# Kernel tuning notes

Hardware: AMD Instinct MI355X
Metric: run time of the kernel (lower is better)

The kernel has to match this reference:

```python
import jax, jax.numpy as jnp
import numpy as np

EMBED_DIM = 512  # channels C
B, H, W = 2, 64, 64


def _conv1x1(x, w, b):
    # x: [B, C, H, W]; w: [C_out, C_in]; b: [C_out]  (1x1 conv == per-pixel linear)
    return jnp.einsum('bchw,dc->bdhw', x, w) + b[None, :, None, None]


def setup_inputs() -> dict:
    key = jax.random.key(0)
    ks = jax.random.split(key, 9)
    C = EMBED_DIM
    s = 1.0 / np.sqrt(C)
    x = jax.random.normal(ks[0], (B, C, H, W), dtype=jnp.float32)
    wq = jax.random.normal(ks[1], (C, C), dtype=jnp.float32) * s
    bq = jax.random.normal(ks[2], (C,), dtype=jnp.float32) * 0.01
    wk = jax.random.normal(ks[3], (C, C), dtype=jnp.float32) * s
    bk = jax.random.normal(ks[4], (C,), dtype=jnp.float32) * 0.01
    wv = jax.random.normal(ks[5], (C, C), dtype=jnp.float32) * s
    bv = jax.random.normal(ks[6], (C,), dtype=jnp.float32) * 0.01
    wo = jax.random.normal(ks[7], (C, C), dtype=jnp.float32) * s
    bo = jax.random.normal(ks[8], (C,), dtype=jnp.float32) * 0.01
    return {"x": x, "wq": wq, "bq": bq, "wk": wk, "bk": bk,
            "wv": wv, "bv": bv, "wo": wo, "bo": bo}


def reference(x, wq, bq, wk, bk, wv, bv, wo, bo):
    b, c, h, w = x.shape
    n = h * w
    q = _conv1x1(x, wq, bq).reshape(b, c, n)
    k = _conv1x1(x, wk, bk).reshape(b, c, n)
    v = _conv1x1(x, wv, bv).reshape(b, c, n)
    # scores = q^T @ k over channel dim -> [b, n, n]; scale by sqrt(C) (scale=True)
    scores = jnp.einsum('bcn,bcm->bnm', q, k) / jnp.sqrt(jnp.asarray(c, x.dtype))
    attn = jax.nn.softmax(scores, axis=-1)
    # output = v @ attn^T -> [b, c, n]
    out = jnp.einsum('bcm,bnm->bcn', v, attn).reshape(b, c, h, w)
    return _conv1x1(out, wo, bo)
```

## Files before the change

### kernel.cpp

```cpp
#include <hip/hip_runtime.h>
#include <stdint.h>

typedef short s16x8 __attribute__((ext_vector_type(8)));
typedef unsigned short u16x8 __attribute__((ext_vector_type(8)));
typedef float f32x4 __attribute__((ext_vector_type(4)));

__device__ __forceinline__ float bf2f(unsigned short u) {
  union { unsigned u; float f; } c; c.u = ((unsigned)u) << 16; return c.f;
}
__device__ __forceinline__ unsigned short f2bf(float f) {
  union { float f; unsigned u; } c; c.f = f;
  unsigned u = c.u + 0x7fffu + ((c.u >> 16) & 1u);
  return (unsigned short)(u >> 16);
}

__device__ __forceinline__ void g2l16(const void* g, void* l) {
  __builtin_amdgcn_global_load_lds(
      (const __attribute__((address_space(1))) void*)(unsigned long long)g,
      (__attribute__((address_space(3))) void*)(unsigned)(unsigned long long)l,
      16, 0, 0);
}

template <int MODE, int MT, int YB>
__global__ __launch_bounds__(2 * MT) void gemm_abt(
    const unsigned short* __restrict__ A, int lda,
    const unsigned short* __restrict__ Bt, int ldb,
    unsigned short* __restrict__ C, int ldc,
    const float* __restrict__ bias,
    float* __restrict__ rowsum,
    int M, int N, int K, int nsplit,
    long long sA, long long sBt, long long sC, long long sSplit,
    float scale)
{
  constexpr int STAGE_ELEMS  = (MT + 128) * 64;
  constexpr int BOUNCE_ELEMS = 128 * 136;
  constexpr int SMEM_ELEMS = STAGE_ELEMS > BOUNCE_ELEMS ? STAGE_ELEMS : BOUNCE_ELEMS;
  __shared__ __align__(16) unsigned short smem[SMEM_ELEMS];
  unsigned short* As = smem;
  unsigned short* Bs = smem + MT * 64;

  const int ks = blockIdx.z % nsplit;
  const int bz = blockIdx.z / nsplit;
  A  += (long long)bz * sA;
  Bt += (long long)bz * sBt;
  C  += (long long)bz * sC + (long long)ks * sSplit;

  int bx, by;
  if (YB > 0) {
    const int lin = blockIdx.x + (int)gridDim.x * blockIdx.y;
    bx = (lin & 7) | ((lin >> (3 + YB)) << 3);
    by = (lin >> 3) & ((1 << YB) - 1);
  } else {
    bx = blockIdx.x;
    by = blockIdx.y;
  }

  const int tile_m = by * MT;
  const int tile_n = bx * 128;

  const int tid  = threadIdx.x;
  const int wid  = tid >> 6;
  const int lane = tid & 63;
  const int wm = (wid >> 1) * 64;
  const int wn = (wid & 1) * 64;
  const int lr = lane & 15;
  const int lq = lane >> 4;

  const int srow = lane >> 3;
  const int scol = ((lane & 7) ^ (srow & 7)) * 8;

  f32x4 acc[4][4];
  const f32x4 zero4 = {0.f, 0.f, 0.f, 0.f};
  #pragma unroll
  for (int i = 0; i < 4; ++i)
    #pragma unroll
    for (int j = 0; j < 4; ++j) acc[i][j] = zero4;

  const unsigned short* Arow = A  + (long long)tile_m * lda;
  const unsigned short* Brow = Bt + (long long)tile_n * ldb;

  const int kLen = K / nsplit;
  const int kBeg = ks * kLen;

  constexpr int ACH   = MT / 8;
  constexpr int NCH   = ACH + 16;
  constexpr int NW    = MT / 32;
  constexpr int PERW  = NCH / NW;

  for (int k0 = kBeg; k0 < kBeg + kLen; k0 += 64) {
    #pragma unroll
    for (int c = 0; c < PERW; ++c) {
      const int chunk = wid * PERW + c;
      if (chunk < ACH) {
        const int row = chunk * 8 + srow;
        g2l16(Arow + (long long)row * lda + k0 + scol, smem + chunk * 512);
      } else {
        const int row = (chunk - ACH) * 8 + srow;
        g2l16(Brow + (long long)row * ldb + k0 + scol, smem + chunk * 512);
      }
    }
    __syncthreads();
    #pragma unroll
    for (int kss = 0; kss < 2; ++kss) {
      const int cch = kss * 4 + lq;
      s16x8 af[4], bfr[4];
      #pragma unroll
      for (int i = 0; i < 4; ++i) {
        const int row = wm + i * 16 + lr;
        af[i] = *(const s16x8*)&As[row * 64 + ((cch ^ (row & 7)) * 8)];
      }
      #pragma unroll
      for (int j = 0; j < 4; ++j) {
        const int row = wn + j * 16 + lr;
        bfr[j] = *(const s16x8*)&Bs[row * 64 + ((cch ^ (row & 7)) * 8)];
      }
      #pragma unroll
      for (int i = 0; i < 4; ++i)
        #pragma unroll
        for (int j = 0; j < 4; ++j)
          acc[i][j] = __builtin_amdgcn_mfma_f32_16x16x32_bf16(af[i], bfr[j], acc[i][j], 0, 0, 0);
    }
    __syncthreads();
  }

  if (MODE == 2) {
    #pragma unroll
    for (int i = 0; i < 4; ++i) {
      float rs[4] = {0.f, 0.f, 0.f, 0.f};
      #pragma unroll
      for (int j = 0; j < 4; ++j)
        #pragma unroll
        for (int r = 0; r < 4; ++r) {
          acc[i][j][r] = __expf(acc[i][j][r] * scale);
          rs[r] += acc[i][j][r];
        }
      #pragma unroll
      for (int r = 0; r < 4; ++r) {
        float s = rs[r];
        s += __shfl_xor(s, 1); s += __shfl_xor(s, 2);
        s += __shfl_xor(s, 4); s += __shfl_xor(s, 8);
        if (lr == 0)
          atomicAdd(&rowsum[(long long)bz * M + tile_m + wm + i * 16 + lq * 4 + r], s);
      }
    }
  }

  if (MT == 128) {
    #pragma unroll
    for (int i = 0; i < 4; ++i) {
      const int lrow0 = wm + i * 16 + lq * 4;
      #pragma unroll
      for (int j = 0; j < 4; ++j) {
        const int lcol = wn + j * 16 + lr;
        const float bcol = (MODE == 1 && bias) ? bias[tile_n + lcol] : 0.f;
        #pragma unroll
        for (int r = 0; r < 4; ++r) {
          const float v = (MODE == 2) ? acc[i][j][r] : acc[i][j][r] * scale + bcol;
          smem[(lrow0 + r) * 136 + lcol] = f2bf(v);
        }
      }
    }
    __syncthreads();
    const int row = tid >> 1;
    const int cb = (tid & 1) * 64;
    #pragma unroll
    for (int k = 0; k < 8; ++k) {
      u16x8 v = *(const u16x8*)&smem[row * 136 + cb + k * 8];
      *(u16x8*)&C[(long long)(tile_m + row) * ldc + tile_n + cb + k * 8] = v;
    }
  } else {
    #pragma unroll
    for (int p = 0; p < 2; ++p) {
      if ((wm >> 7) == p) {
        const int lwm = wm & 127;
        #pragma unroll
        for (int i = 0; i < 4; ++i) {
          const int lrow0 = lwm + i * 16 + lq * 4;
          #pragma unroll
          for (int j = 0; j < 4; ++j) {
            const int lcol = wn + j * 16 + lr;
            const float bcol = (MODE == 1 && bias) ? bias[tile_n + lcol] : 0.f;
            #pragma unroll
            for (int r = 0; r < 4; ++r) {
              const float v = (MODE == 2) ? acc[i][j][r] : acc[i][j][r] * scale + bcol;
              smem[(lrow0 + r) * 136 + lcol] = f2bf(v);
            }
          }
        }
      }
      __syncthreads();
      if ((tid >> 8) == p) {
        const int t2 = tid & 255;
        const int row = t2 >> 1;
        const int cb = (t2 & 1) * 64;
        #pragma unroll
        for (int k = 0; k < 8; ++k) {
          u16x8 v = *(const u16x8*)&smem[row * 136 + cb + k * 8];
          *(u16x8*)&C[(long long)(tile_m + p * 128 + row) * ldc + tile_n + cb + k * 8] = v;
        }
      }
      if (p == 0) __syncthreads();
    }
  }
}

__global__ __launch_bounds__(256) void cvt_weights(
    const float* __restrict__ wq, const float* __restrict__ wk,
    const float* __restrict__ wv, const float* __restrict__ wo,
    const float* __restrict__ bq, const float* __restrict__ bk,
    const float* __restrict__ bv, const float* __restrict__ bo,
    unsigned short* __restrict__ W3, unsigned short* __restrict__ wvT_b,
    unsigned short* __restrict__ wo_b, float* __restrict__ bqk3,
    float* __restrict__ bpp, float* __restrict__ rowsum, int n)
{
  if ((int)blockIdx.x < 1024) {
    const int i = blockIdx.x * 256 + threadIdx.x;
    if (i < n) {
      W3[i]      = f2bf(wq[i]);
      W3[n + i]  = f2bf(wk[i]);
      wvT_b[i]   = f2bf(wv[(i & 511) * 512 + (i >> 9)]);
      wo_b[i]    = f2bf(wo[i]);
    }
    if (i < 512) {
      bqk3[i]        = bq[i];
      bqk3[512 + i]  = bk[i];
      bqk3[1024 + i] = 0.f;
    }
    if (i < 8192) rowsum[i] = 0.f;
  } else {
    const int w = threadIdx.x >> 6, lane = threadIdx.x & 63;
    const int d = (blockIdx.x - 1024) * 4 + w;
    const float* row = wo + (long long)d * 512;
    float s = 0.f;
    #pragma unroll
    for (int c = 0; c < 512; c += 64) s += row[c + lane] * bv[c + lane];
    #pragma unroll
    for (int o = 32; o > 0; o >>= 1) s += __shfl_xor(s, o, 64);
    if (lane == 0) bpp[d] = s + bo[d];
  }
}

__global__ __launch_bounds__(256) void transpose_cn(
    const float* __restrict__ x, unsigned short* __restrict__ xT,
    int C, int N)
{
  __shared__ float tile[32][33];
  const long long boff = (long long)blockIdx.z * C * N;
  const int n0 = blockIdx.x * 32;
  const int c0 = blockIdx.y * 32;
  const int tx = threadIdx.x;
  const int ty = threadIdx.y;
  #pragma unroll
  for (int k = 0; k < 32; k += 8)
    tile[ty + k][tx] = x[boff + (long long)(c0 + ty + k) * N + n0 + tx];
  __syncthreads();
  #pragma unroll
  for (int k = 0; k < 32; k += 8)
    xT[boff + (long long)(n0 + ty + k) * C + c0 + tx] = f2bf(tile[tx][ty + k]);
}

__global__ __launch_bounds__(256) void transpose_bf(
    const unsigned short* __restrict__ src, int srcLd, long long sSrc,
    unsigned short* __restrict__ dst, int dstLd, long long sDst,
    int R, int Cc)
{
  __shared__ unsigned short tile[32][33];
  const int r0 = blockIdx.x * 32;
  const int c0 = blockIdx.y * 32;
  const int tx = threadIdx.x;
  const int ty = threadIdx.y;
  const long long so = (long long)blockIdx.z * sSrc;
  const long long dofs = (long long)blockIdx.z * sDst;
  #pragma unroll
  for (int k = 0; k < 32; k += 8)
    tile[ty + k][tx] = src[so + (long long)(r0 + ty + k) * srcLd + c0 + tx];
  __syncthreads();
  #pragma unroll
  for (int k = 0; k < 32; k += 8)
    dst[dofs + (long long)(c0 + ty + k) * dstLd + r0 + tx] = tile[tx][ty + k];
}

__global__ __launch_bounds__(256) void reduce4_norm_out(
    const unsigned short* __restrict__ p, long long L,
    const float* __restrict__ rowsum, const float* __restrict__ bpp,
    float* __restrict__ o)
{
  const long long i = 8LL * (blockIdx.x * 256 + threadIdx.x);
  const int b = (int)(i >> 21);
  const int d = (int)((i >> 12) & 511);
  const int n = (int)(i & 4095);
  const float bb = bpp[d];
  const float* rs = &rowsum[b * 4096 + n];
  u16x8 a  = *(const u16x8*)&p[i];
  u16x8 b1 = *(const u16x8*)&p[L + i];
  u16x8 c  = *(const u16x8*)&p[2 * L + i];
  u16x8 d1 = *(const u16x8*)&p[3 * L + i];
  f32x4 o0, o1;
  #pragma unroll
  for (int j = 0; j < 4; ++j) {
    o0[j] = ((bf2f(a[j]) + bf2f(b1[j])) + (bf2f(c[j]) + bf2f(d1[j]))) / rs[j] + bb;
    o1[j] = ((bf2f(a[4 + j]) + bf2f(b1[4 + j])) + (bf2f(c[4 + j]) + bf2f(d1[4 + j]))) / rs[4 + j] + bb;
  }
  *(f32x4*)&o[i] = o0;
  *(f32x4*)&o[i + 4] = o1;
}

extern "C" void kernel_launch(void* const* d_in, const int* in_sizes, int n_in,
                              void* d_out, int out_size, void* d_ws, size_t ws_size,
                              hipStream_t stream) {
  (void)in_sizes; (void)n_in; (void)out_size; (void)ws_size;
  const float* x  = (const float*)d_in[0];
  const float* wq = (const float*)d_in[1];
  const float* bq = (const float*)d_in[2];
  const float* wk = (const float*)d_in[3];
  const float* bk = (const float*)d_in[4];
  const float* wv = (const float*)d_in[5];
  const float* bv = (const float*)d_in[6];
  const float* wo = (const float*)d_in[7];
  const float* bo = (const float*)d_in[8];
  float* out = (float*)d_out;

  const int Cc = 512, N = 4096, Bn = 2, C3 = 1536;
  const int CC = Cc * Cc;
  const long long NC  = (long long)N * Cc;
  const long long NC3 = (long long)N * C3;
  const long long NN  = (long long)N * N;

  char* wsb = (char*)d_ws;
  unsigned short* W3    = (unsigned short*)wsb;
  unsigned short* wvT_b = W3 + 3LL * CC;
  unsigned short* wo_b  = wvT_b + CC;
  float*          bqk3  = (float*)(wo_b + CC);
  float*          bpp   = bqk3 + 1536;
  float*          rsum  = bpp + 512;
  unsigned short* xT    = (unsigned short*)(rsum + 8192);
  unsigned short* qkvoT = xT + Bn * NC;
  unsigned short* vo    = qkvoT + Bn * NC3;
  unsigned short* S     = vo + Bn * NC;
  unsigned short* part  = S + Bn * NN;

  const float inv_sqrt_c = 0.044194173824159216f;

  cvt_weights<<<dim3(1152), 256, 0, stream>>>(
      wq, wk, wv, wo, bq, bk, bv, bo, W3, wvT_b, wo_b, bqk3, bpp, rsum, CC);
  gemm_abt<1, 128, 0><<<dim3(4, 4, 1), 256, 0, stream>>>(
      wo_b, 512, wvT_b, 512, W3 + 2LL * CC, 512, nullptr, nullptr,
      512, 512, 512, 1, 0, 0, 0, 0, 1.0f);
  transpose_cn<<<dim3(N / 32, Cc / 32, Bn), dim3(32, 8), 0, stream>>>(x, xT, Cc, N);

  gemm_abt<1, 256, 0><<<dim3(C3 / 128, N / 256, Bn), 512, 0, stream>>>(
      xT, Cc, W3, Cc, qkvoT, C3, bqk3, nullptr, N, C3, Cc, 1,
      NC, 0, NC3, 0, 1.0f);
  transpose_bf<<<dim3(N / 32, Cc / 32, Bn), dim3(32, 8), 0, stream>>>(
      qkvoT + 1024, C3, NC3, vo, N, NC, N, Cc);
  gemm_abt<2, 256, 4><<<dim3(N / 128, N / 256, Bn), 512, 0, stream>>>(
      qkvoT, C3, qkvoT + 512, C3, S, N, nullptr, rsum, N, N, Cc, 1,
      NC3, NC3, NN, 0, inv_sqrt_c);
  gemm_abt<1, 256, 1><<<dim3(N / 128, 512 / 256, Bn * 4), 512, 0, stream>>>(
      vo, N, S, N, part, N, nullptr, nullptr, 512, N, N, 4,
      NC, NN, NC, (long long)Bn * NC, 1.0f);
  reduce4_norm_out<<<dim3((int)((Bn * NC) / 2048)), 256, 0, stream>>>(
      part, (long long)Bn * NC, rsum, bpp, out);
}
```

Before: 240.3 us.

## Fuse V transpose into QKV GEMM epilogue and merge prep kernels

The QKV projection GEMM gets a new mode in which tiles covering the V columns are written transposed, through shared memory, straight into the channel-major V buffer. This removes the separate bf16 transpose kernel and its extra read and write of V. The weight conversion and the x transpose are merged into one prep kernel, which saves a launch. Q and K now go to a narrower buffer with stride 1024, and the V tiles skip the bias, which is folded into bpp downstream.

```diff
diff --git a/kernel.cpp b/kernel.cpp
--- a/kernel.cpp
+++ b/kernel.cpp
@@ -3,6 +3,7 @@
 
 typedef short s16x8 __attribute__((ext_vector_type(8)));
 typedef unsigned short u16x8 __attribute__((ext_vector_type(8)));
+typedef unsigned short u16x4 __attribute__((ext_vector_type(4)));
 typedef float f32x4 __attribute__((ext_vector_type(4)));
 
 __device__ __forceinline__ float bf2f(unsigned short u) {
@@ -30,7 +31,8 @@
     float* __restrict__ rowsum,
     int M, int N, int K, int nsplit,
     long long sA, long long sBt, long long sC, long long sSplit,
-    float scale)
+    float scale,
+    unsigned short* __restrict__ C2, int ldc2, long long sC2)
 {
   constexpr int STAGE_ELEMS  = (MT + 128) * 64;
   constexpr int BOUNCE_ELEMS = 128 * 136;
@@ -123,6 +125,42 @@
     __syncthreads();
   }
 
+
+  if (MODE == 3 && bx >= 8) {
+    const int tile_d0 = (bx - 8) * 128;
+    unsigned short* V = C2 + (long long)bz * sC2;
+    #pragma unroll
+    for (int p = 0; p < 2; ++p) {
+      if ((wid & 1) == p) {
+        #pragma unroll
+        for (int j = 0; j < 4; ++j) {
+          const int dl = j * 16 + lr;
+          #pragma unroll
+          for (int i = 0; i < 4; ++i) {
+            const int nbase = wm + i * 16 + lq * 4;
+            u16x4 w4;
+            #pragma unroll
+            for (int r = 0; r < 4; ++r) w4[r] = f2bf(acc[i][j][r]);
+            *(u16x4*)&smem[dl * 264 + nbase] = w4;
+          }
+        }
+      }
+      __syncthreads();
+      {
+        const int dl = tid >> 3;
+        const int nb = (tid & 7) * 32;
+        unsigned short* dst = V + (long long)(tile_d0 + p * 64 + dl) * ldc2 + tile_m + nb;
+        #pragma unroll
+        for (int k = 0; k < 4; ++k) {
+          u16x8 v = *(const u16x8*)&smem[dl * 264 + nb + k * 8];
+          *(u16x8*)&dst[k * 8] = v;
+        }
+      }
+      if (p == 0) __syncthreads();
+    }
+    return;
+  }
+
   if (MODE == 2) {
     #pragma unroll
     for (int i = 0; i < 4; ++i) {
@@ -152,7 +190,7 @@
       #pragma unroll
       for (int j = 0; j < 4; ++j) {
         const int lcol = wn + j * 16 + lr;
-        const float bcol = (MODE == 1 && bias) ? bias[tile_n + lcol] : 0.f;
+        const float bcol = ((MODE == 1 || MODE == 3) && bias) ? bias[tile_n + lcol] : 0.f;
         #pragma unroll
         for (int r = 0; r < 4; ++r) {
           const float v = (MODE == 2) ? acc[i][j][r] : acc[i][j][r] * scale + bcol;
@@ -179,7 +217,7 @@
           #pragma unroll
           for (int j = 0; j < 4; ++j) {
             const int lcol = wn + j * 16 + lr;
-            const float bcol = (MODE == 1 && bias) ? bias[tile_n + lcol] : 0.f;
+            const float bcol = ((MODE == 1 || MODE == 3) && bias) ? bias[tile_n + lcol] : 0.f;
             #pragma unroll
             for (int r = 0; r < 4; ++r) {
               const float v = (MODE == 2) ? acc[i][j][r] : acc[i][j][r] * scale + bcol;
@@ -204,32 +242,31 @@
   }
 }
 
-__global__ __launch_bounds__(256) void cvt_weights(
+__global__ __launch_bounds__(256) void prep(
+    const float* __restrict__ x,
     const float* __restrict__ wq, const float* __restrict__ wk,
     const float* __restrict__ wv, const float* __restrict__ wo,
     const float* __restrict__ bq, const float* __restrict__ bk,
     const float* __restrict__ bv, const float* __restrict__ bo,
     unsigned short* __restrict__ W3, unsigned short* __restrict__ wvT_b,
-    unsigned short* __restrict__ wo_b, float* __restrict__ bqk3,
-    float* __restrict__ bpp, float* __restrict__ rowsum, int n)
+    unsigned short* __restrict__ wo_b, unsigned short* __restrict__ xT,
+    float* __restrict__ bqk, float* __restrict__ bpp,
+    float* __restrict__ rowsum)
 {
-  if ((int)blockIdx.x < 1024) {
-    const int i = blockIdx.x * 256 + threadIdx.x;
-    if (i < n) {
-      W3[i]      = f2bf(wq[i]);
-      W3[n + i]  = f2bf(wk[i]);
-      wvT_b[i]   = f2bf(wv[(i & 511) * 512 + (i >> 9)]);
-      wo_b[i]    = f2bf(wo[i]);
-    }
-    if (i < 512) {
-      bqk3[i]        = bq[i];
-      bqk3[512 + i]  = bk[i];
-      bqk3[1024 + i] = 0.f;
-    }
+  __shared__ float tile[32][33];
+  const int lin = blockIdx.x;
+  const int tid = threadIdx.x;
+  if (lin < 1024) {
+    const int i = lin * 256 + tid;
+    W3[i]          = f2bf(wq[i]);
+    W3[262144 + i] = f2bf(wk[i]);
+    wvT_b[i]       = f2bf(wv[(i & 511) * 512 + (i >> 9)]);
+    wo_b[i]        = f2bf(wo[i]);
+    if (i < 512) { bqk[i] = bq[i]; bqk[512 + i] = bk[i]; }
     if (i < 8192) rowsum[i] = 0.f;
-  } else {
-    const int w = threadIdx.x >> 6, lane = threadIdx.x & 63;
-    const int d = (blockIdx.x - 1024) * 4 + w;
+  } else if (lin < 1152) {
+    const int w = tid >> 6, lane = tid & 63;
+    const int d = (lin - 1024) * 4 + w;
     const float* row = wo + (long long)d * 512;
     float s = 0.f;
     #pragma unroll
@@ -237,47 +274,21 @@
     #pragma unroll
     for (int o = 32; o > 0; o >>= 1) s += __shfl_xor(s, o, 64);
     if (lane == 0) bpp[d] = s + bo[d];
-  }
-}
-
-__global__ __launch_bounds__(256) void transpose_cn(
-    const float* __restrict__ x, unsigned short* __restrict__ xT,
-    int C, int N)
-{
-  __shared__ float tile[32][33];
-  const long long boff = (long long)blockIdx.z * C * N;
-  const int n0 = blockIdx.x * 32;
-  const int c0 = blockIdx.y * 32;
-  const int tx = threadIdx.x;
-  const int ty = threadIdx.y;
-  #pragma unroll
-  for (int k = 0; k < 32; k += 8)
-    tile[ty + k][tx] = x[boff + (long long)(c0 + ty + k) * N + n0 + tx];
-  __syncthreads();
-  #pragma unroll
-  for (int k = 0; k < 32; k += 8)
-    xT[boff + (long long)(n0 + ty + k) * C + c0 + tx] = f2bf(tile[tx][ty + k]);
-}
-
-__global__ __launch_bounds__(256) void transpose_bf(
-    const unsigned short* __restrict__ src, int srcLd, long long sSrc,
-    unsigned short* __restrict__ dst, int dstLd, long long sDst,
-    int R, int Cc)
-{
-  __shared__ unsigned short tile[32][33];
-  const int r0 = blockIdx.x * 32;
-  const int c0 = blockIdx.y * 32;
-  const int tx = threadIdx.x;
-  const int ty = threadIdx.y;
-  const long long so = (long long)blockIdx.z * sSrc;
-  const long long dofs = (long long)blockIdx.z * sDst;
-  #pragma unroll
-  for (int k = 0; k < 32; k += 8)
-    tile[ty + k][tx] = src[so + (long long)(r0 + ty + k) * srcLd + c0 + tx];
-  __syncthreads();
-  #pragma unroll
-  for (int k = 0; k < 32; k += 8)
-    dst[dofs + (long long)(c0 + ty + k) * dstLd + r0 + tx] = tile[tx][ty + k];
+  } else {
+    const int t = lin - 1152;
+    const int n0 = (t & 127) * 32;
+    const int c0 = ((t >> 7) & 15) * 32;
+    const int bz = t >> 11;
+    const int tx = tid & 31, ty = tid >> 5;
+    const long long boff = (long long)bz * (512LL * 4096);
+    #pragma unroll
+    for (int k = 0; k < 32; k += 8)
+      tile[ty + k][tx] = x[boff + (long long)(c0 + ty + k) * 4096 + n0 + tx];
+    __syncthreads();
+    #pragma unroll
+    for (int k = 0; k < 32; k += 8)
+      xT[boff + (long long)(n0 + ty + k) * 512 + c0 + tx] = f2bf(tile[tx][ty + k]);
+  }
 }
 
 __global__ __launch_bounds__(256) void reduce4_norm_out(
@@ -320,45 +331,41 @@
   const float* bo = (const float*)d_in[8];
   float* out = (float*)d_out;
 
-  const int Cc = 512, N = 4096, Bn = 2, C3 = 1536;
+  const int Cc = 512, N = 4096, Bn = 2;
   const int CC = Cc * Cc;
   const long long NC  = (long long)N * Cc;
-  const long long NC3 = (long long)N * C3;
+  const long long NK  = (long long)N * 1024;
   const long long NN  = (long long)N * N;
 
   char* wsb = (char*)d_ws;
   unsigned short* W3    = (unsigned short*)wsb;
   unsigned short* wvT_b = W3 + 3LL * CC;
   unsigned short* wo_b  = wvT_b + CC;
-  float*          bqk3  = (float*)(wo_b + CC);
-  float*          bpp   = bqk3 + 1536;
+  float*          bqk   = (float*)(wo_b + CC);
+  float*          bpp   = bqk + 1024;
   float*          rsum  = bpp + 512;
   unsigned short* xT    = (unsigned short*)(rsum + 8192);
-  unsigned short* qkvoT = xT + Bn * NC;
-  unsigned short* vo    = qkvoT + Bn * NC3;
+  unsigned short* qkT   = xT + Bn * NC;
+  unsigned short* vo    = qkT + Bn * NK;
   unsigned short* S     = vo + Bn * NC;
   unsigned short* part  = S + Bn * NN;
 
   const float inv_sqrt_c = 0.044194173824159216f;
 
-  cvt_weights<<<dim3(1152), 256, 0, stream>>>(
-      wq, wk, wv, wo, bq, bk, bv, bo, W3, wvT_b, wo_b, bqk3, bpp, rsum, CC);
+  prep<<<dim3(1152 + 128 * 16 * Bn), 256, 0, stream>>>(
+      x, wq, wk, wv, wo, bq, bk, bv, bo, W3, wvT_b, wo_b, xT, bqk, bpp, rsum);
   gemm_abt<1, 128, 0><<<dim3(4, 4, 1), 256, 0, stream>>>(
       wo_b, 512, wvT_b, 512, W3 + 2LL * CC, 512, nullptr, nullptr,
-      512, 512, 512, 1, 0, 0, 0, 0, 1.0f);
-  transpose_cn<<<dim3(N / 32, Cc / 32, Bn), dim3(32, 8), 0, stream>>>(x, xT, Cc, N);
-
-  gemm_abt<1, 256, 0><<<dim3(C3 / 128, N / 256, Bn), 512, 0, stream>>>(
-      xT, Cc, W3, Cc, qkvoT, C3, bqk3, nullptr, N, C3, Cc, 1,
-      NC, 0, NC3, 0, 1.0f);
-  transpose_bf<<<dim3(N / 32, Cc / 32, Bn), dim3(32, 8), 0, stream>>>(
-      qkvoT + 1024, C3, NC3, vo, N, NC, N, Cc);
+      512, 512, 512, 1, 0, 0, 0, 0, 1.0f, nullptr, 0, 0);
+  gemm_abt<3, 256, 0><<<dim3(12, N / 256, Bn), 512, 0, stream>>>(
+      xT, Cc, W3, Cc, qkT, 1024, bqk, nullptr, N, 1536, Cc, 1,
+      NC, 0, NK, 0, 1.0f, vo, N, NC);
   gemm_abt<2, 256, 4><<<dim3(N / 128, N / 256, Bn), 512, 0, stream>>>(
-      qkvoT, C3, qkvoT + 512, C3, S, N, nullptr, rsum, N, N, Cc, 1,
-      NC3, NC3, NN, 0, inv_sqrt_c);
+      qkT, 1024, qkT + 512, 1024, S, N, nullptr, rsum, N, N, Cc, 1,
+      NK, NK, NN, 0, inv_sqrt_c, nullptr, 0, 0);
   gemm_abt<1, 256, 1><<<dim3(N / 128, 512 / 256, Bn * 4), 512, 0, stream>>>(
       vo, N, S, N, part, N, nullptr, nullptr, 512, N, N, 4,
-      NC, NN, NC, (long long)Bn * NC, 1.0f);
+      NC, NN, NC, (long long)Bn * NC, 1.0f, nullptr, 0, 0);
   reduce4_norm_out<<<dim3((int)((Bn * NC) / 2048)), 256, 0, stream>>>(
       part, (long long)Bn * NC, rsum, bpp, out);
 }
```

After: 254.5 us. 1.06x slower.
